# Kernel optimization log

Measured on AMD Instinct MI355X. Metric: run time of the kernel, lower is better.

## Reference

```python
import jax, jax.numpy as jnp
import numpy as np


def setup_inputs() -> dict:
    key = jax.random.key(0)
    k1, k2 = jax.random.split(key)
    B, N, M = 8, 4096, 4096
    points1 = jax.random.normal(k1, (B, N, 3), dtype=jnp.float32)
    points2 = jax.random.normal(k2, (B, M, 3), dtype=jnp.float32)
    return {"points1": points1, "points2": points2}


def reference(points1, points2):
    x2 = jnp.sum(points1 * points1, axis=-1)            # [B, N]
    y2 = jnp.sum(points2 * points2, axis=-1)            # [B, M]
    xy = jnp.einsum('bnd,bmd->bnm', points1, points2)   # [B, N, M]
    d = x2[:, :, None] + y2[:, None, :] - 2.0 * xy      # [B, N, M]
    dist1 = jnp.min(d, axis=2)                          # [B, N] NN dist p1->p2
    dist2 = jnp.min(d, axis=1)                          # [B, M] NN dist p2->p1
    # Symmetric Hausdorff: max over each direction, then max of the two, sum over batch
    m = jnp.maximum(jnp.max(dist1, axis=-1), jnp.max(dist2, axis=-1))  # [B]
    return jnp.sum(m)
```

## Files before the change

### kernel.cpp

```cpp
#include <hip/hip_runtime.h>
#include <float.h>

#define B_CONST 8
#define GROUPS 8
#define QSPLIT 8

typedef float v2f __attribute__((ext_vector_type(2)));

__device__ __forceinline__ v2f pk_fma(v2f a, v2f b, v2f c) {
    v2f d;
    asm("v_pk_fma_f32 %0, %1, %2, %3" : "=v"(d) : "v"(a), "v"(b), "v"(c));
    return d;
}
__device__ __forceinline__ float min3(float a, float b, float c) {
    float d;
    asm("v_min3_f32 %0, %1, %2, %3" : "=v"(d) : "v"(a), "v"(b), "v"(c));
    return d;
}

__global__ __launch_bounds__(256) void hd_nnmax(
    const float* __restrict__ p1raw, const float* __restrict__ p2raw,
    float* __restrict__ part, unsigned int* __restrict__ comm,
    int N, int M, int blocksDir0) {
    int blk = blockIdx.x;
    if (blk == 0 && threadIdx.x < 9) comm[threadIdx.x] = 0u;

    const float* qraw; const float* rraw; int QN, RM, dir;
    if (blk < blocksDir0) { qraw = p1raw; rraw = p2raw; QN = N; RM = M; dir = 0; }
    else { blk -= blocksDir0; qraw = p2raw; rraw = p1raw; QN = M; RM = N; dir = 1; }

    int qblocks = QN >> 9;
    int perB = qblocks * GROUPS;
    int b    = blk / perB;
    int rem  = blk - b * perB;
    int qblk = rem / GROUPS;
    int g    = rem - qblk * GROUPS;

    int l = threadIdx.x & 63;
    int w = __builtin_amdgcn_readfirstlane((int)(threadIdx.x >> 6));

    __shared__ float buf[2048];
    __shared__ float qw_s[512];

    int refsPerGroup = RM / GROUPS;
    const float* rsrc = rraw + 3 * ((size_t)b * RM + (size_t)g * refsPerGroup);
    {
        int i = threadIdx.x;
        float x0 = rsrc[6*i],   y0 = rsrc[6*i+1], z0 = rsrc[6*i+2];
        float x1 = rsrc[6*i+3], y1 = rsrc[6*i+4], z1 = rsrc[6*i+5];
        float* t = buf + 8 * i;
        t[0] = -2.0f * x0; t[1] = -2.0f * x1;
        t[2] = -2.0f * y0; t[3] = -2.0f * y1;
        t[4] = -2.0f * z0; t[5] = -2.0f * z1;
        t[6] = fmaf(x0, x0, fmaf(y0, y0, z0 * z0));
        t[7] = fmaf(x1, x1, fmaf(y1, y1, z1 * z1));
    }

    const float* qb = qraw + 3 * ((size_t)b * QN + ((size_t)qblk << 9));
    v2f QX[8], QY[8], QZ[8];
    float MN[8];
    #pragma unroll
    for (int s = 0; s < 8; ++s) {
        int q = s * 64 + l;
        float x = qb[3*q], y = qb[3*q+1], z = qb[3*q+2];
        QX[s] = (v2f){ x, x };
        QY[s] = (v2f){ y, y };
        QZ[s] = (v2f){ z, z };
        MN[s] = FLT_MAX;
        if (w == 0) qw_s[q] = fmaf(x, x, fmaf(y, y, z * z));
    }
    __syncthreads();

    const v2f* lp = (const v2f*)buf + (size_t)(w * 64) * 4;
    #pragma unroll 4
    for (int j = 0; j < 64; ++j) {
        v2f RX = lp[4*j + 0];
        v2f RY = lp[4*j + 1];
        v2f RZ = lp[4*j + 2];
        v2f RW = lp[4*j + 3];
        #pragma unroll
        for (int s = 0; s < 8; ++s) {
            v2f a = pk_fma(QX[s], RX, RW);
            a = pk_fma(QY[s], RY, a);
            a = pk_fma(QZ[s], RZ, a);
            MN[s] = min3(MN[s], a.x, a.y);
        }
    }
    __syncthreads();

    #pragma unroll
    for (int s = 0; s < 8; ++s)
        buf[(w << 9) + s * 64 + l] = MN[s];
    __syncthreads();

    size_t dirOff = dir ? (size_t)GROUPS * B_CONST * N : 0;
    float* pb = part + dirOff + ((size_t)g * B_CONST + b) * QN + ((size_t)qblk << 9);
    for (int t = threadIdx.x; t < 512; t += 256) {
        float m = fminf(fminf(buf[t], buf[512 + t]),
                        fminf(buf[1024 + t], buf[1536 + t]));
        pb[t] = fmaxf(qw_s[t] + m, 0.0f);
    }
}

__global__ __launch_bounds__(256) void hd_final(
    const float* __restrict__ part, unsigned int* __restrict__ comm,
    float* __restrict__ out, int N, int M) {
    int db  = blockIdx.x >> 3;
    int qs  = blockIdx.x & (QSPLIT - 1);
    int dir = db >> 3;
    int b   = db & 7;
    int QN  = dir ? M : N;
    size_t dirOff = dir ? (size_t)GROUPS * B_CONST * N : 0;
    const float* fb = part + dirOff + (size_t)b * QN;
    size_t gs = (size_t)B_CONST * QN;

    int span = QN / QSPLIT;
    int q0 = qs * span;
    float mx = 0.0f;
    for (int qq = q0 + threadIdx.x; qq < q0 + span; qq += 256) {
        float mm = fb[qq];
        #pragma unroll
        for (int gg = 1; gg < GROUPS; ++gg)
            mm = fminf(mm, fb[(size_t)gg * gs + qq]);
        mx = fmaxf(mx, mm);
    }
    #pragma unroll
    for (int off = 32; off > 0; off >>= 1)
        mx = fmaxf(mx, __shfl_down(mx, off, 64));
    __shared__ float wred[4];
    int l = threadIdx.x & 63, w = threadIdx.x >> 6;
    if (l == 0) wred[w] = mx;
    __syncthreads();
    if (threadIdx.x == 0) {
        mx = fmaxf(fmaxf(wred[0], wred[1]), fmaxf(wred[2], wred[3]));
        atomicMax(&comm[b], __float_as_uint(mx));
        __threadfence();
        unsigned int t2 = atomicAdd(&comm[8], 1u);
        if (t2 == (unsigned int)(16 * QSPLIT - 1)) {
            float s = 0.0f;
            for (int bb = 0; bb < B_CONST; ++bb)
                s += __uint_as_float(atomicMax(&comm[bb], 0u));
            out[0] = s;
        }
    }
}

extern "C" void kernel_launch(void* const* d_in, const int* in_sizes, int n_in,
                              void* d_out, int out_size, void* d_ws, size_t ws_size,
                              hipStream_t stream) {
    const float* p1 = (const float*)d_in[0];
    const float* p2 = (const float*)d_in[1];
    const int B = B_CONST;
    int N = in_sizes[0] / (3 * B);
    int M = in_sizes[1] / (3 * B);
    int n1 = B * N, n2 = B * M;

    char* ws = (char*)d_ws;
    float* part = (float*)ws;
    unsigned int* comm = (unsigned int*)(part + (size_t)GROUPS * (n1 + n2));

    int blocksDir0 = B * (N >> 9) * GROUPS;
    int blocksDir1 = B * (M >> 9) * GROUPS;
    hd_nnmax<<<blocksDir0 + blocksDir1, 256, 0, stream>>>(
        p1, p2, part, comm, N, M, blocksDir0);

    hd_final<<<16 * QSPLIT, 256, 0, stream>>>(part, comm, (float*)d_out, N, M);
}
```

Before: 82.66 us.

## Compute pairwise distances with split-bf16 MFMA and fuse both NN directions

Replaces the packed-FMA distance loop with bf16 MFMA 16x16x32. Each point is split into high and low bf16 parts, with norms folded into the K dimension, so the MFMA output is the full squared distance at roughly fp32 accuracy. Each tile now yields both row minima (shuffle reductions) and column minima (LDS atomicMin). This drops the second pass over the transposed problem and halves the distance work. The risks are precision loss from the bf16 split, LDS atomic contention on every MFMA step, and a larger column partial buffer for the final kernel to reduce.

```diff
diff --git a/kernel.cpp b/kernel.cpp
--- a/kernel.cpp
+++ b/kernel.cpp
@@ -2,15 +2,17 @@
 #include <float.h>
 
 #define B_CONST 8
-#define GROUPS 8
-#define QSPLIT 8
+#define ONE_BF 0x3F80
 
-typedef float v2f __attribute__((ext_vector_type(2)));
+typedef short short8 __attribute__((ext_vector_type(8)));
+typedef float f32x4  __attribute__((ext_vector_type(4)));
 
-__device__ __forceinline__ v2f pk_fma(v2f a, v2f b, v2f c) {
-    v2f d;
-    asm("v_pk_fma_f32 %0, %1, %2, %3" : "=v"(d) : "v"(a), "v"(b), "v"(c));
-    return d;
+__device__ __forceinline__ unsigned short f2bf(float f) {
+    unsigned u = __float_as_uint(f);
+    return (unsigned short)((u + 0x7FFFu + ((u >> 16) & 1u)) >> 16);
+}
+__device__ __forceinline__ float bf2f(unsigned short h) {
+    return __uint_as_float(((unsigned)h) << 16);
 }
 __device__ __forceinline__ float min3(float a, float b, float c) {
     float d;
@@ -18,110 +20,143 @@
     return d;
 }
 
-__global__ __launch_bounds__(256) void hd_nnmax(
-    const float* __restrict__ p1raw, const float* __restrict__ p2raw,
-    float* __restrict__ part, unsigned int* __restrict__ comm,
-    int N, int M, int blocksDir0) {
+__global__ __launch_bounds__(256) void hd_mfma(
+    const float* __restrict__ p1, const float* __restrict__ p2,
+    float* __restrict__ part_row, float* __restrict__ part_col,
+    unsigned int* __restrict__ comm, int N, int M) {
+    int t = threadIdx.x;
     int blk = blockIdx.x;
-    if (blk == 0 && threadIdx.x < 9) comm[threadIdx.x] = 0u;
+    if (blk == 0 && t < 9) comm[t] = 0u;
 
-    const float* qraw; const float* rraw; int QN, RM, dir;
-    if (blk < blocksDir0) { qraw = p1raw; rraw = p2raw; QN = N; RM = M; dir = 0; }
-    else { blk -= blocksDir0; qraw = p2raw; rraw = p1raw; QN = M; RM = N; dir = 1; }
+    int gCount  = M >> 10;
+    int rbCount = N >> 7;
+    int perB = rbCount * gCount;
+    int b   = blk / perB;
+    int rem = blk - b * perB;
+    int rb  = rem / gCount;
+    int g   = rem - rb * gCount;
 
-    int qblocks = QN >> 9;
-    int perB = qblocks * GROUPS;
-    int b    = blk / perB;
-    int rem  = blk - b * perB;
-    int qblk = rem / GROUPS;
-    int g    = rem - qblk * GROUPS;
+    __shared__ unsigned short ldsBlo[8192];
+    __shared__ unsigned short ldsBhi[8192];
+    __shared__ unsigned short ldsA0[1024];
+    __shared__ unsigned short ldsA1[512];
+    __shared__ unsigned int   ldsColU[1024];
+    __shared__ float          ldsRow[128];
+    __shared__ unsigned short ldsZero[8];
 
-    int l = threadIdx.x & 63;
-    int w = __builtin_amdgcn_readfirstlane((int)(threadIdx.x >> 6));
+    if (t < 8) ldsZero[t] = 0;
+    for (int i = t; i < 1024; i += 256) ldsColU[i] = 0x7F7FFFFFu;
 
-    __shared__ float buf[2048];
-    __shared__ float qw_s[512];
-
-    int refsPerGroup = RM / GROUPS;
-    const float* rsrc = rraw + 3 * ((size_t)b * RM + (size_t)g * refsPerGroup);
-    {
-        int i = threadIdx.x;
-        float x0 = rsrc[6*i],   y0 = rsrc[6*i+1], z0 = rsrc[6*i+2];
-        float x1 = rsrc[6*i+3], y1 = rsrc[6*i+4], z1 = rsrc[6*i+5];
-        float* t = buf + 8 * i;
-        t[0] = -2.0f * x0; t[1] = -2.0f * x1;
-        t[2] = -2.0f * y0; t[3] = -2.0f * y1;
-        t[4] = -2.0f * z0; t[5] = -2.0f * z1;
-        t[6] = fmaf(x0, x0, fmaf(y0, y0, z0 * z0));
-        t[7] = fmaf(x1, x1, fmaf(y1, y1, z1 * z1));
+    const float* rsrc = p2 + 3 * ((size_t)b * M + ((size_t)g << 10));
+    for (int i = t; i < 1024; i += 256) {
+        float x = rsrc[3*i], y = rsrc[3*i+1], z = rsrc[3*i+2];
+        unsigned short hx = f2bf(x), hy = f2bf(y), hz = f2bf(z);
+        float ex = x - bf2f(hx), ey = y - bf2f(hy), ez = z - bf2f(hz);
+        unsigned short m2ex = f2bf(-2.f*ex), m2ey = f2bf(-2.f*ey), m2ez = f2bf(-2.f*ez);
+        float rw = fmaf(x,x,fmaf(y,y,z*z));
+        unsigned short hrw = f2bf(rw);
+        unsigned short erw = f2bf(rw - bf2f(hrw));
+        unsigned* lo = (unsigned*)(ldsBlo + i*8);
+        lo[0] = hx | ((unsigned)hy << 16);
+        lo[1] = hz | ((unsigned)hx << 16);
+        lo[2] = hy | ((unsigned)hz << 16);
+        lo[3] = m2ex | ((unsigned)m2ey << 16);
+        unsigned* hi = (unsigned*)(ldsBhi + i*8);
+        hi[0] = m2ez | ((unsigned)hrw << 16);
+        hi[1] = erw | ((unsigned)ONE_BF << 16);
+        hi[2] = ONE_BF;
+        hi[3] = 0;
     }
-
-    const float* qb = qraw + 3 * ((size_t)b * QN + ((size_t)qblk << 9));
-    v2f QX[8], QY[8], QZ[8];
-    float MN[8];
-    #pragma unroll
-    for (int s = 0; s < 8; ++s) {
-        int q = s * 64 + l;
-        float x = qb[3*q], y = qb[3*q+1], z = qb[3*q+2];
-        QX[s] = (v2f){ x, x };
-        QY[s] = (v2f){ y, y };
-        QZ[s] = (v2f){ z, z };
-        MN[s] = FLT_MAX;
-        if (w == 0) qw_s[q] = fmaf(x, x, fmaf(y, y, z * z));
+    const float* qsrc = p1 + 3 * ((size_t)b * N + ((size_t)rb << 7));
+    if (t < 128) {
+        float x = qsrc[3*t], y = qsrc[3*t+1], z = qsrc[3*t+2];
+        unsigned short hx = f2bf(x), hy = f2bf(y), hz = f2bf(z);
+        float ex = x - bf2f(hx), ey = y - bf2f(hy), ez = z - bf2f(hz);
+        float qw = fmaf(x,x,fmaf(y,y,z*z));
+        unsigned short hqw = f2bf(qw);
+        unsigned short eqw = f2bf(qw - bf2f(hqw));
+        unsigned* a0 = (unsigned*)(ldsA0 + t*8);
+        a0[0] = f2bf(-2.f*bf2f(hx)) | ((unsigned)f2bf(-2.f*bf2f(hy)) << 16);
+        a0[1] = f2bf(-2.f*bf2f(hz)) | ((unsigned)f2bf(-2.f*ex) << 16);
+        a0[2] = f2bf(-2.f*ey) | ((unsigned)f2bf(-2.f*ez) << 16);
+        a0[3] = hx | ((unsigned)hy << 16);
+        unsigned* a1 = (unsigned*)(ldsA1 + t*4);
+        a1[0] = hz | ((unsigned)hqw << 16);
+        a1[1] = eqw;
     }
     __syncthreads();
 
-    const v2f* lp = (const v2f*)buf + (size_t)(w * 64) * 4;
-    #pragma unroll 4
-    for (int j = 0; j < 64; ++j) {
-        v2f RX = lp[4*j + 0];
-        v2f RY = lp[4*j + 1];
-        v2f RZ = lp[4*j + 2];
-        v2f RW = lp[4*j + 3];
+    int l = t & 63, w = t >> 6;
+    int n = l & 15, quad = l >> 4;
+    const unsigned short* bbase = (quad == 0) ? (ldsBlo + n*8)
+                                : (quad == 1) ? (ldsBhi + n*8) : ldsZero;
+    int bstride = (quad < 2) ? 128 : 0;
+
+    f32x4 zacc = {0.f, 0.f, 0.f, 0.f};
+
+    for (int s = w; s < 8; s += 4) {
+        int qhat = (s << 4) + n;
+        short8 af;
+        {
+            short8 a0v = *(const short8*)(ldsA0 + qhat*8);
+            unsigned short hz_ = ldsA1[qhat*4], hqw = ldsA1[qhat*4+1], eqw = ldsA1[qhat*4+2];
+            short8 ahi = { (short)hz_, (short)ONE_BF, (short)ONE_BF,
+                           (short)hqw, (short)eqw, 0, 0, 0 };
+            short8 az = {0,0,0,0,0,0,0,0};
+            af = (quad == 0) ? a0v : (quad == 1) ? ahi : az;
+        }
+        float rm0 = FLT_MAX, rm1 = FLT_MAX, rm2 = FLT_MAX, rm3 = FLT_MAX;
+        #pragma unroll 4
+        for (int j = 0; j < 64; ++j) {
+            short8 bf = *(const short8*)(bbase + j * bstride);
+            f32x4 D = __builtin_amdgcn_mfma_f32_16x16x32_bf16(af, bf, zacc, 0, 0, 0);
+            rm0 = fminf(rm0, D[0]); rm1 = fminf(rm1, D[1]);
+            rm2 = fminf(rm2, D[2]); rm3 = fminf(rm3, D[3]);
+            float cm = fminf(min3(D[0], D[1], D[2]), D[3]);
+            atomicMin(&ldsColU[(j << 4) + n], __float_as_uint(cm));
+        }
         #pragma unroll
-        for (int s = 0; s < 8; ++s) {
-            v2f a = pk_fma(QX[s], RX, RW);
-            a = pk_fma(QY[s], RY, a);
-            a = pk_fma(QZ[s], RZ, a);
-            MN[s] = min3(MN[s], a.x, a.y);
+        for (int msk = 1; msk < 16; msk <<= 1) {
+            rm0 = fminf(rm0, __shfl_xor(rm0, msk, 64));
+            rm1 = fminf(rm1, __shfl_xor(rm1, msk, 64));
+            rm2 = fminf(rm2, __shfl_xor(rm2, msk, 64));
+            rm3 = fminf(rm3, __shfl_xor(rm3, msk, 64));
+        }
+        if (n == 0) {
+            float* rr = ldsRow + (s << 4) + (quad << 2);
+            rr[0] = rm0; rr[1] = rm1; rr[2] = rm2; rr[3] = rm3;
         }
     }
     __syncthreads();
 
-    #pragma unroll
-    for (int s = 0; s < 8; ++s)
-        buf[(w << 9) + s * 64 + l] = MN[s];
-    __syncthreads();
-
-    size_t dirOff = dir ? (size_t)GROUPS * B_CONST * N : 0;
-    float* pb = part + dirOff + ((size_t)g * B_CONST + b) * QN + ((size_t)qblk << 9);
-    for (int t = threadIdx.x; t < 512; t += 256) {
-        float m = fminf(fminf(buf[t], buf[512 + t]),
-                        fminf(buf[1024 + t], buf[1536 + t]));
-        pb[t] = fmaxf(qw_s[t] + m, 0.0f);
-    }
+    if (t < 128)
+        part_row[((size_t)g * B_CONST + b) * N + ((size_t)rb << 7) + t] =
+            fmaxf(ldsRow[t], 0.f);
+    for (int i = t; i < 1024; i += 256)
+        part_col[((size_t)b * rbCount + rb) * M + ((size_t)g << 10) + i] =
+            fmaxf(__uint_as_float(ldsColU[i]), 0.f);
 }
 
 __global__ __launch_bounds__(256) void hd_final(
-    const float* __restrict__ part, unsigned int* __restrict__ comm,
-    float* __restrict__ out, int N, int M) {
+    const float* __restrict__ part_row, const float* __restrict__ part_col,
+    unsigned int* __restrict__ comm, float* __restrict__ out, int N, int M) {
     int db  = blockIdx.x >> 3;
-    int qs  = blockIdx.x & (QSPLIT - 1);
+    int qs  = blockIdx.x & 7;
     int dir = db >> 3;
-    int b   = db & 7;
+    int bb  = db & 7;
+    int G   = dir ? (N >> 7) : (M >> 10);
     int QN  = dir ? M : N;
-    size_t dirOff = dir ? (size_t)GROUPS * B_CONST * N : 0;
-    const float* fb = part + dirOff + (size_t)b * QN;
-    size_t gs = (size_t)B_CONST * QN;
+    const float* base = dir ? part_col + (size_t)bb * (N >> 7) * M
+                            : part_row + (size_t)bb * N;
+    size_t gstride = dir ? (size_t)M : (size_t)B_CONST * N;
 
-    int span = QN / QSPLIT;
+    int span = QN >> 3;
     int q0 = qs * span;
-    float mx = 0.0f;
+    float mx = 0.f;
     for (int qq = q0 + threadIdx.x; qq < q0 + span; qq += 256) {
-        float mm = fb[qq];
-        #pragma unroll
-        for (int gg = 1; gg < GROUPS; ++gg)
-            mm = fminf(mm, fb[(size_t)gg * gs + qq]);
+        float mm = base[qq];
+        for (int gg = 1; gg < G; ++gg)
+            mm = fminf(mm, base[(size_t)gg * gstride + qq]);
         mx = fmaxf(mx, mm);
     }
     #pragma unroll
@@ -133,13 +168,13 @@
     __syncthreads();
     if (threadIdx.x == 0) {
         mx = fmaxf(fmaxf(wred[0], wred[1]), fmaxf(wred[2], wred[3]));
-        atomicMax(&comm[b], __float_as_uint(mx));
+        atomicMax(&comm[bb], __float_as_uint(mx));
         __threadfence();
         unsigned int t2 = atomicAdd(&comm[8], 1u);
-        if (t2 == (unsigned int)(16 * QSPLIT - 1)) {
-            float s = 0.0f;
-            for (int bb = 0; bb < B_CONST; ++bb)
-                s += __uint_as_float(atomicMax(&comm[bb], 0u));
+        if (t2 == 127u) {
+            float s = 0.f;
+            for (int k = 0; k < B_CONST; ++k)
+                s += __uint_as_float(atomicMax(&comm[k], 0u));
             out[0] = s;
         }
     }
@@ -153,16 +188,12 @@
     const int B = B_CONST;
     int N = in_sizes[0] / (3 * B);
     int M = in_sizes[1] / (3 * B);
-    int n1 = B * N, n2 = B * M;
 
-    char* ws = (char*)d_ws;
-    float* part = (float*)ws;
-    unsigned int* comm = (unsigned int*)(part + (size_t)GROUPS * (n1 + n2));
+    float* part_row = (float*)d_ws;
+    float* part_col = part_row + (size_t)(M >> 10) * B * N;
+    unsigned int* comm = (unsigned int*)(part_col + (size_t)(N >> 7) * B * M);
 
-    int blocksDir0 = B * (N >> 9) * GROUPS;
-    int blocksDir1 = B * (M >> 9) * GROUPS;
-    hd_nnmax<<<blocksDir0 + blocksDir1, 256, 0, stream>>>(
-        p1, p2, part, comm, N, M, blocksDir0);
-
-    hd_final<<<16 * QSPLIT, 256, 0, stream>>>(part, comm, (float*)d_out, N, M);
+    int blocks = B * (N >> 7) * (M >> 10);
+    hd_mfma<<<blocks, 256, 0, stream>>>(p1, p2, part_row, part_col, comm, N, M);
+    hd_final<<<128, 256, 0, stream>>>(part_row, part_col, comm, (float*)d_out, N, M);
 }
```

Result: slower. 96.66 us (+16.9%).
